# Kernel optimization log

Hardware: AMD Instinct MI355X
Metric: run time of the kernel (lower is better)

The kernel has to match this reference:

```python
import jax, jax.numpy as jnp
import numpy as np

N_POINTS = 1_500_000
N_SUPERPOINTS = 50_000
FEAT_DIM = 32
HIDDEN_DIM = 64
EMBED_DIM = 128


def setup_inputs() -> dict:
    key = jax.random.key(0)
    k1, k2, k3, k4, k5, k6 = jax.random.split(key, 6)
    return {
        "full_features": jax.random.normal(k1, (N_POINTS, FEAT_DIM), dtype=jnp.float32),
        "super_indices": jax.random.randint(k2, (N_POINTS,), 0, N_SUPERPOINTS, dtype=jnp.int64)
        if jax.config.jax_enable_x64 else jax.random.randint(k2, (N_POINTS,), 0, N_SUPERPOINTS, dtype=jnp.int32),
        "W1": jax.random.normal(k3, (FEAT_DIM, HIDDEN_DIM), dtype=jnp.float32) * 0.1,
        "b1": jax.random.normal(k4, (HIDDEN_DIM,), dtype=jnp.float32) * 0.01,
        "W2": jax.random.normal(k5, (HIDDEN_DIM, EMBED_DIM), dtype=jnp.float32) * 0.1,
        "b2": jax.random.normal(k6, (EMBED_DIM,), dtype=jnp.float32) * 0.01,
    }


def reference(full_features, super_indices, W1, b1, W2, b2):
    # Fused gather -> 2-layer MLP -> per-superpoint max reduction.
    # Equivalent to SuperPointNet.gen_token_embed, vectorized over all
    # superpoints instead of a Python loop with boolean-mask gathers.
    h = jax.nn.relu(full_features @ W1 + b1)          # [N, HIDDEN]
    h = jax.nn.relu(h @ W2 + b2)                      # [N, EMBED]
    sp_features = jax.ops.segment_max(
        h, super_indices, num_segments=N_SUPERPOINTS, indices_are_sorted=False
    )                                                  # [NS, EMBED]
    # Guard empty superpoints (segment_max yields -inf); original loop
    # assumes every superpoint id is present.
    sp_features = jnp.where(jnp.isfinite(sp_features), sp_features, 0.0)
    return sp_features
```

## Files before the change

kernel.cpp:

```cpp
#include <hip/hip_runtime.h>
#include <hip/hip_bf16.h>


#define NPTS 1500000
#define NSEG 50000
#define CAP  120
#define CAPX 64

typedef __attribute__((ext_vector_type(8))) short short8;
typedef __attribute__((ext_vector_type(4))) float floatx4;
typedef __attribute__((ext_vector_type(2))) float floatx2;
typedef __attribute__((ext_vector_type(4))) unsigned int uintx4;

__device__ __forceinline__ unsigned short f2bf(float f) {
    unsigned int x = __float_as_uint(f);
    x += 0x7FFFu + ((x >> 16) & 1u);
    return (unsigned short)(x >> 16);
}
__device__ __forceinline__ float bf2f(unsigned short b) {
    return __uint_as_float(((unsigned int)b) << 16);
}
__device__ __forceinline__ unsigned cvt_pk_bf16(float lo, float hi) {
    unsigned r;
    asm("v_cvt_pk_bf16_f32 %0, %1, %2" : "=v"(r) : "v"(lo), "v"(hi));
    return r;
}

__device__ __forceinline__ short8 load_x(const void* Xv, int pid, int quad, int isbf)
{
    if (isbf) {
        return *(const short8*)((const unsigned short*)Xv + (size_t)pid * 32 + quad * 8);
    } else {
        const float* xf = (const float*)Xv + (size_t)pid * 32 + quad * 8;
        const floatx4 f0 = *(const floatx4*)xf;
        const floatx4 f1 = *(const floatx4*)(xf + 4);
        union { short8 s; unsigned u[4]; } a;
        a.u[0] = cvt_pk_bf16(f0[0], f0[1]);
        a.u[1] = cvt_pk_bf16(f0[2], f0[3]);
        a.u[2] = cvt_pk_bf16(f1[0], f1[1]);
        a.u[3] = cvt_pk_bf16(f1[2], f1[3]);
        return a.s;
    }
}

__device__ __forceinline__ int probe_idx64(const unsigned* idxw, unsigned* scnt)
{
    __syncthreads();
    if (threadIdx.x == 0) *scnt = 0u;
    __syncthreads();
    int nz = 0;
    #pragma unroll
    for (int j = 0; j < 2; ++j)
        nz += (idxw[(threadIdx.x * 2 + j) * 2 + 1] != 0u) ? 1 : 0;
    atomicAdd(scnt, (unsigned)nz);
    __syncthreads();
    return (*scnt < 256u) ? 1 : 0;
}

__device__ __forceinline__ int probe_isbf(const unsigned* Xw, unsigned* scnt)
{
    __syncthreads();
    if (threadIdx.x == 0) *scnt = 0u;
    __syncthreads();
    int c = 0;
    #pragma unroll
    for (int j = 0; j < 4; ++j) {
        unsigned u  = Xw[threadIdx.x * 4 + j];
        unsigned he = (u >> 23) & 0xFFu, le = (u >> 7) & 0xFFu;
        c += (he >= 100u && he <= 140u && le >= 100u && le <= 140u) ? 1 : 0;
    }
    atomicAdd(scnt, (unsigned)c);
    __syncthreads();
    return (*scnt >= 512u) ? 1 : 0;
}

__device__ __forceinline__ void load_row(const unsigned* Xw, int i, int isbf, uintx4 r[4])
{
    if (isbf) {
        const uintx4* s = (const uintx4*)((const char*)Xw + (size_t)i * 64);
        r[0] = s[0]; r[1] = s[1]; r[2] = s[2]; r[3] = s[3];
    } else {
        const floatx4* f = (const floatx4*)((const char*)Xw + (size_t)i * 128);
        #pragma unroll
        for (int k = 0; k < 4; ++k) {
            const floatx4 a = f[2 * k], b = f[2 * k + 1];
            uintx4 w;
            w[0] = cvt_pk_bf16(a[0], a[1]);
            w[1] = cvt_pk_bf16(a[2], a[3]);
            w[2] = cvt_pk_bf16(b[0], b[1]);
            w[3] = cvt_pk_bf16(b[2], b[3]);
            r[k] = w;
        }
    }
}

__global__ __launch_bounds__(256)
void build_rows(const unsigned* __restrict__ idxw,
                const unsigned* __restrict__ Xw,
                unsigned* __restrict__ cnt,
                int* __restrict__ slots,
                unsigned short* __restrict__ Xs,
                unsigned* __restrict__ flags)
{
    __shared__ unsigned sc;
    const int idx64 = probe_idx64(idxw, &sc);
    const int isbf  = probe_isbf(Xw, &sc);
    if (blockIdx.x == 0 && threadIdx.x == 0) flags[0] = (unsigned)isbf;

    const int S  = gridDim.x * 256;
    const int i0 = blockIdx.x * 256 + threadIdx.x;
    const int i1 = i0 + S;

    unsigned s0 = 0xFFFFFFFFu, s1 = 0xFFFFFFFFu;
    if (i0 < NPTS) s0 = idx64 ? idxw[2 * (size_t)i0] : idxw[i0];
    if (i1 < NPTS) s1 = idx64 ? idxw[2 * (size_t)i1] : idxw[i1];

    uintx4 r0[4], r1[4];
    if (s0 < NSEG) load_row(Xw, i0, isbf, r0);
    if (s1 < NSEG) load_row(Xw, i1, isbf, r1);

    unsigned p0 = 0, p1 = 0;
    if (s0 < NSEG) p0 = atomicAdd(&cnt[s0], 1u);
    if (s1 < NSEG) p1 = atomicAdd(&cnt[s1], 1u);

    if (s0 < NSEG) {
        if (p0 < CAP)  slots[(size_t)s0 * CAP + p0] = i0;
        if (p0 < CAPX) {
            uintx4* d = (uintx4*)(Xs + ((size_t)s0 * CAPX + p0) * 32);
            d[0] = r0[0]; d[1] = r0[1]; d[2] = r0[2]; d[3] = r0[3];
        }
    }
    if (s1 < NSEG) {
        if (p1 < CAP)  slots[(size_t)s1 * CAP + p1] = i1;
        if (p1 < CAPX) {
            uintx4* d = (uintx4*)(Xs + ((size_t)s1 * CAPX + p1) * 32);
            d[0] = r1[0]; d[1] = r1[1]; d[2] = r1[2]; d[3] = r1[3];
        }
    }
}

__device__ __forceinline__ void tile_mlp(const short8 acur,
                                         const short8 w1f[4],
                                         const short8 w2f[2][8],
                                         const float b1v[16],
                                         const float b2v[8],
                                         float vmax[8],
                                         const int quad,
                                         const int lim, const bool full)
{
    floatx4 c1[4];
    #pragma unroll
    for (int t = 0; t < 4; ++t) {
        floatx4 z = {0.f, 0.f, 0.f, 0.f};
        c1[t] = __builtin_amdgcn_mfma_f32_16x16x32_bf16(w1f[t], acur, z, 0, 0, 0);
    }

    union { short8 s; unsigned u[4]; } af0, af1;
    #pragma unroll
    for (int t = 0; t < 4; ++t) {
        const float h0 = fmaxf(c1[t][0] + b1v[t * 4 + 0], 0.f);
        const float h1 = fmaxf(c1[t][1] + b1v[t * 4 + 1], 0.f);
        const float h2 = fmaxf(c1[t][2] + b1v[t * 4 + 2], 0.f);
        const float h3 = fmaxf(c1[t][3] + b1v[t * 4 + 3], 0.f);
        const unsigned lo = cvt_pk_bf16(h0, h1);
        const unsigned hi = cvt_pk_bf16(h2, h3);
        if (t == 0)      { af0.u[0] = lo; af0.u[1] = hi; }
        else if (t == 1) { af0.u[2] = lo; af0.u[3] = hi; }
        else if (t == 2) { af1.u[0] = lo; af1.u[1] = hi; }
        else             { af1.u[2] = lo; af1.u[3] = hi; }
    }

    #pragma unroll
    for (int t = 0; t < 8; ++t) {
        floatx4 c4 = {0.f, 0.f, 0.f, 0.f};
        c4 = __builtin_amdgcn_mfma_f32_16x16x32_bf16(af0.s, w2f[0][t], c4, 0, 0, 0);
        c4 = __builtin_amdgcn_mfma_f32_16x16x32_bf16(af1.s, w2f[1][t], c4, 0, 0, 0);
        #pragma unroll
        for (int r = 0; r < 4; ++r) {
            const float v = c4[r] + b2v[t];
            vmax[t] = fmaxf(vmax[t], (full || (quad * 4 + r) < lim) ? v : 0.f);
        }
    }
}

__device__ __forceinline__ short8 row_tile(const unsigned short* Xs, int seg,
                                           int ti, int l16, int quad)
{
    return *(const short8*)(Xs + ((size_t)seg * CAPX + ti * 16 + l16) * 32 + quad * 8);
}

template<int DT>
__global__ __launch_bounds__(256)
void seg_mlp_rows(const void* __restrict__ Xv,
                  const void* __restrict__ W1v, const void* __restrict__ B1v,
                  const void* __restrict__ W2v, const void* __restrict__ B2v,
                  const unsigned* __restrict__ cnt,
                  const int* __restrict__ slots,
                  const unsigned short* __restrict__ Xs,
                  const unsigned* __restrict__ flags,
                  void* __restrict__ outv)
{
    if (flags[0] != (unsigned)DT) return;

    __shared__ __align__(16) float outs[4][128];

    const int tid = threadIdx.x, wave = tid >> 6, lane = tid & 63;
    const int quad = lane >> 4, l16 = lane & 15;

    short8 w1f[4];
    #pragma unroll
    for (int t = 0; t < 4; ++t)
        #pragma unroll
        for (int j = 0; j < 8; ++j) {
            const int e = (quad * 8 + j) * 64 + t * 16 + l16;
            w1f[t][j] = DT ? (short)((const unsigned short*)W1v)[e]
                           : (short)f2bf(((const float*)W1v)[e]);
        }

    short8 w2f[2][8];
    #pragma unroll
    for (int kt = 0; kt < 2; ++kt)
        #pragma unroll
        for (int t = 0; t < 8; ++t)
            #pragma unroll
            for (int j = 0; j < 8; ++j) {
                const int k = kt * 32 + (j >> 2) * 16 + quad * 4 + (j & 3);
                const int e = k * 128 + t * 16 + l16;
                w2f[kt][t][j] = DT ? (short)((const unsigned short*)W2v)[e]
                                   : (short)f2bf(((const float*)W2v)[e]);
            }

    float b1v[16];
    #pragma unroll
    for (int t = 0; t < 4; ++t)
        #pragma unroll
        for (int r = 0; r < 4; ++r) {
            const int n = t * 16 + quad * 4 + r;
            b1v[t * 4 + r] = DT ? bf2f(((const unsigned short*)B1v)[n])
                                : ((const float*)B1v)[n];
        }
    float b2v[8];
    #pragma unroll
    for (int t = 0; t < 8; ++t)
        b2v[t] = DT ? bf2f(((const unsigned short*)B2v)[t * 16 + l16])
                    : ((const float*)B2v)[t * 16 + l16];

    float* fs = outs[wave];
    const int gw = blockIdx.x * 4 + wave, nw = gridDim.x * 4;

    unsigned c_cur = 0;
    short8 r0 = {}, r1 = {};
    if (gw < NSEG) {
        c_cur = cnt[gw];
        r0 = row_tile(Xs, gw, 0, l16, quad);
        r1 = row_tile(Xs, gw, 1, l16, quad);
    }

    for (int seg = gw; seg < NSEG; seg += nw) {
        const int c_raw = (int)c_cur;
        const int c  = min(c_raw, CAPX);
        const int nt = (c + 15) >> 4;

        short8 r2 = {}, r3 = {};
        if (nt > 2) r2 = row_tile(Xs, seg, 2, l16, quad);
        if (nt > 3) r3 = row_tile(Xs, seg, 3, l16, quad);

        const int segn = seg + nw;
        unsigned cn = 0;
        short8 r0n = {}, r1n = {};
        if (segn < NSEG) {
            cn  = cnt[segn];
            r0n = row_tile(Xs, segn, 0, l16, quad);
            r1n = row_tile(Xs, segn, 1, l16, quad);
        }

        float vmax[8];
        #pragma unroll
        for (int t = 0; t < 8; ++t) vmax[t] = 0.f;

        if (c_raw > CAPX) {
            const int c2 = min(c_raw, CAP);
            const int nt2 = (c2 + 15) >> 4, last = c2 - 1;
            const size_t base = (size_t)seg * CAP;
            for (int ti = 0; ti < nt2; ++ti) {
                int pid = slots[base + min(ti * 16 + l16, last)];
                pid = min(max(pid, 0), NPTS - 1);
                const short8 acur = load_x(Xv, pid, quad, DT);
                tile_mlp(acur, w1f, w2f, b1v, b2v, vmax, quad, 16, true);
            }
        } else if (c > 0) {
            #pragma unroll
            for (int ti = 0; ti < 4; ++ti) {
                if (ti < nt) {
                    const short8 acur = (ti == 0) ? r0 : (ti == 1) ? r1
                                      : (ti == 2) ? r2 : r3;
                    const int lim = c - ti * 16;
                    tile_mlp(acur, w1f, w2f, b1v, b2v, vmax, quad,
                             lim, lim >= 16);
                }
            }
        }

        #pragma unroll
        for (int t = 0; t < 8; ++t) {
            vmax[t] = fmaxf(vmax[t], __shfl_xor(vmax[t], 16, 64));
            vmax[t] = fmaxf(vmax[t], __shfl_xor(vmax[t], 32, 64));
        }
        if (quad == 0) {
            #pragma unroll
            for (int t = 0; t < 8; ++t) fs[t * 16 + l16] = vmax[t];
        }
        __builtin_amdgcn_s_waitcnt(0xC07F);
        const floatx2 o2 = ((const floatx2*)fs)[lane];
        if (DT) {
            ((unsigned*)outv)[seg * 64 + lane] = cvt_pk_bf16(o2[0], o2[1]);
        } else {
            ((floatx2*)outv)[seg * 64 + lane] = o2;
        }
        __builtin_amdgcn_s_waitcnt(0xC07F);

        c_cur = cn; r0 = r0n; r1 = r1n;
    }
}

__global__ __launch_bounds__(256)
void build_slots(const unsigned* __restrict__ idxw,
                 const unsigned* __restrict__ Xw,
                 unsigned* __restrict__ cnt,
                 int* __restrict__ slots,
                 unsigned* __restrict__ flags)
{
    __shared__ unsigned sc;
    const int idx64 = probe_idx64(idxw, &sc);

    if (blockIdx.x == 0) {
        const int isbf = probe_isbf(Xw, &sc);
        if (threadIdx.x == 0) flags[0] = (unsigned)isbf;
    }

    const int S  = gridDim.x * 256;
    const int i0 = blockIdx.x * 256 + threadIdx.x;
    const int i1 = i0 + S, i2 = i1 + S;

    unsigned s0 = 0xFFFFFFFFu, s1 = 0xFFFFFFFFu, s2 = 0xFFFFFFFFu;
    if (i0 < NPTS) s0 = idx64 ? idxw[2 * (size_t)i0] : idxw[i0];
    if (i1 < NPTS) s1 = idx64 ? idxw[2 * (size_t)i1] : idxw[i1];
    if (i2 < NPTS) s2 = idx64 ? idxw[2 * (size_t)i2] : idxw[i2];

    unsigned p0 = 0, p1 = 0, p2 = 0;
    if (s0 < NSEG) p0 = atomicAdd(&cnt[s0], 1u);
    if (s1 < NSEG) p1 = atomicAdd(&cnt[s1], 1u);
    if (s2 < NSEG) p2 = atomicAdd(&cnt[s2], 1u);

    if (s0 < NSEG && p0 < CAP) slots[(size_t)s0 * CAP + p0] = i0;
    if (s1 < NSEG && p1 < CAP) slots[(size_t)s1 * CAP + p1] = i1;
    if (s2 < NSEG && p2 < CAP) slots[(size_t)s2 * CAP + p2] = i2;
}

template<int DT>
__global__ __launch_bounds__(256)
void seg_mlp_max(const void* __restrict__ Xv,
                 const void* __restrict__ W1v, const void* __restrict__ B1v,
                 const void* __restrict__ W2v, const void* __restrict__ B2v,
                 const unsigned* __restrict__ cnt,
                 const int* __restrict__ slots,
                 const unsigned* __restrict__ flags,
                 void* __restrict__ outv)
{
    if (flags[0] != (unsigned)DT) return;

    __shared__ __align__(16) float outs[4][128];

    const int tid = threadIdx.x, wave = tid >> 6, lane = tid & 63;
    const int quad = lane >> 4, l16 = lane & 15;

    short8 w1f[4];
    #pragma unroll
    for (int t = 0; t < 4; ++t)
        #pragma unroll
        for (int j = 0; j < 8; ++j) {
            const int e = (quad * 8 + j) * 64 + t * 16 + l16;
            w1f[t][j] = DT ? (short)((const unsigned short*)W1v)[e]
                           : (short)f2bf(((const float*)W1v)[e]);
        }
    short8 w2f[2][8];
    #pragma unroll
    for (int kt = 0; kt < 2; ++kt)
        #pragma unroll
        for (int t = 0; t < 8; ++t)
            #pragma unroll
            for (int j = 0; j < 8; ++j) {
                const int k = kt * 32 + (j >> 2) * 16 + quad * 4 + (j & 3);
                const int e = k * 128 + t * 16 + l16;
                w2f[kt][t][j] = DT ? (short)((const unsigned short*)W2v)[e]
                                   : (short)f2bf(((const float*)W2v)[e]);
            }
    float b1v[16];
    #pragma unroll
    for (int t = 0; t < 4; ++t)
        #pragma unroll
        for (int r = 0; r < 4; ++r) {
            const int n = t * 16 + quad * 4 + r;
            b1v[t * 4 + r] = DT ? bf2f(((const unsigned short*)B1v)[n])
                                : ((const float*)B1v)[n];
        }
    float b2v[8];
    #pragma unroll
    for (int t = 0; t < 8; ++t)
        b2v[t] = DT ? bf2f(((const unsigned short*)B2v)[t * 16 + l16])
                    : ((const float*)B2v)[t * 16 + l16];

    float* fs = outs[wave];
    const int gw = blockIdx.x * 4 + wave, nw = gridDim.x * 4;

    for (int seg = gw; seg < NSEG; seg += nw) {
        const int c = min((int)cnt[seg], CAP);

        float vmax[8];
        #pragma unroll
        for (int t = 0; t < 8; ++t) vmax[t] = 0.f;

        if (c > 0) {
            const int nt = (c + 15) >> 4, last = c - 1;
            const size_t base = (size_t)seg * CAP;

            short8 abuf[2];
            abuf[0] = load_x(Xv, slots[base + min(l16, last)], quad, DT);
            if (nt > 1)
                abuf[1] = load_x(Xv, slots[base + min(16 + l16, last)], quad, DT);

            for (int ti = 0; ti < nt; ++ti) {
                const short8 acur = abuf[ti & 1];
                if (ti + 2 < nt)
                    abuf[ti & 1] = load_x(
                        Xv, slots[base + min((ti + 2) * 16 + l16, last)], quad, DT);
                tile_mlp(acur, w1f, w2f, b1v, b2v, vmax, quad, 16, true);
            }
        }

        #pragma unroll
        for (int t = 0; t < 8; ++t) {
            vmax[t] = fmaxf(vmax[t], __shfl_xor(vmax[t], 16, 64));
            vmax[t] = fmaxf(vmax[t], __shfl_xor(vmax[t], 32, 64));
        }
        if (quad == 0) {
            #pragma unroll
            for (int t = 0; t < 8; ++t) fs[t * 16 + l16] = vmax[t];
        }
        __builtin_amdgcn_s_waitcnt(0xC07F);
        const floatx2 o2 = ((const floatx2*)fs)[lane];
        if (DT) {
            ((unsigned*)outv)[seg * 64 + lane] = cvt_pk_bf16(o2[0], o2[1]);
        } else {
            ((floatx2*)outv)[seg * 64 + lane] = o2;
        }
        __builtin_amdgcn_s_waitcnt(0xC07F);
    }
}

extern "C" void kernel_launch(void* const* d_in, const int* in_sizes, int n_in,
                              void* d_out, int out_size, void* d_ws, size_t ws_size,
                              hipStream_t stream)
{
    const void* X   = d_in[0];
    const void* idx = d_in[1];
    const void* W1  = d_in[2];
    const void* B1  = d_in[3];
    const void* W2  = d_in[4];
    const void* B2  = d_in[5];

    char* w = (char*)d_ws;
    unsigned* cnt   = (unsigned*)w;  w += ((size_t)NSEG * 4 + 63) & ~63ull;
    unsigned* flags = (unsigned*)w;  w += 64;
    int*      slots = (int*)w;       w += (size_t)NSEG * CAP * 4;
    unsigned short* Xs = (unsigned short*)w;

    const size_t need_fast =
        (((size_t)NSEG * 4 + 63) & ~63ull) + 64 +
        (size_t)NSEG * CAP * 4 + (size_t)NSEG * CAPX * 64;

    hipMemsetAsync(cnt, 0, (size_t)NSEG * 4, stream);

    if (ws_size >= need_fast) {
        build_rows<<<3072, 256, 0, stream>>>((const unsigned*)idx, (const unsigned*)X,
                                             cnt, slots, Xs, flags);
        seg_mlp_rows<1><<<4096, 256, 0, stream>>>(X, W1, B1, W2, B2, cnt, slots,
                                                  Xs, flags, d_out);
        seg_mlp_rows<0><<<4096, 256, 0, stream>>>(X, W1, B1, W2, B2, cnt, slots,
                                                  Xs, flags, d_out);
    } else {
        build_slots<<<2048, 256, 0, stream>>>((const unsigned*)idx, (const unsigned*)X,
                                              cnt, slots, flags);
        seg_mlp_max<1><<<4096, 256, 0, stream>>>(X, W1, B1, W2, B2, cnt, slots,
                                                 flags, d_out);
        seg_mlp_max<0><<<4096, 256, 0, stream>>>(X, W1, B1, W2, B2, cnt, slots,
                                                 flags, d_out);
    }
}
```

Baseline: 449.3 us.

## Pad per-segment counters to 128B lines and prefetch all four row tiles

Segment counters are spread so each occupies its own 128-byte line, so the atomic increments in the scatter kernel no longer hit the same cache line as neighbouring segments. The MLP kernel now prefetches all four staged row tiles of the next segment unconditionally, instead of two tiles ahead plus two on demand, to hide load latency. The cost is a larger workspace and a bigger counter memset, plus extra loads of unused tiles for small segments.

Result: no change. 456.3 us (+1.5%).

```diff
diff --git a/kernel.cpp b/kernel.cpp
--- a/kernel.cpp
+++ b/kernel.cpp
@@ -100,7 +100,8 @@
                 unsigned* __restrict__ cnt,
                 int* __restrict__ slots,
                 unsigned short* __restrict__ Xs,
-                unsigned* __restrict__ flags)
+                unsigned* __restrict__ flags,
+                const int csh)
 {
     __shared__ unsigned sc;
     const int idx64 = probe_idx64(idxw, &sc);
@@ -120,8 +121,8 @@
     if (s1 < NSEG) load_row(Xw, i1, isbf, r1);
 
     unsigned p0 = 0, p1 = 0;
-    if (s0 < NSEG) p0 = atomicAdd(&cnt[s0], 1u);
-    if (s1 < NSEG) p1 = atomicAdd(&cnt[s1], 1u);
+    if (s0 < NSEG) p0 = atomicAdd(&cnt[(size_t)s0 << csh], 1u);
+    if (s1 < NSEG) p1 = atomicAdd(&cnt[(size_t)s1 << csh], 1u);
 
     if (s0 < NSEG) {
         if (p0 < CAP)  slots[(size_t)s0 * CAP + p0] = i0;
@@ -198,7 +199,8 @@
                   const int* __restrict__ slots,
                   const unsigned short* __restrict__ Xs,
                   const unsigned* __restrict__ flags,
-                  void* __restrict__ outv)
+                  void* __restrict__ outv,
+                  const int csh)
 {
     if (flags[0] != (unsigned)DT) return;
 
@@ -249,30 +251,30 @@
     const int gw = blockIdx.x * 4 + wave, nw = gridDim.x * 4;
 
     unsigned c_cur = 0;
-    short8 r0 = {}, r1 = {};
+    short8 t0 = {}, t1 = {}, t2 = {}, t3 = {};
     if (gw < NSEG) {
-        c_cur = cnt[gw];
-        r0 = row_tile(Xs, gw, 0, l16, quad);
-        r1 = row_tile(Xs, gw, 1, l16, quad);
+        c_cur = cnt[(size_t)gw << csh];
+        t0 = row_tile(Xs, gw, 0, l16, quad);
+        t1 = row_tile(Xs, gw, 1, l16, quad);
+        t2 = row_tile(Xs, gw, 2, l16, quad);
+        t3 = row_tile(Xs, gw, 3, l16, quad);
     }
 
     for (int seg = gw; seg < NSEG; seg += nw) {
+        const int segn = seg + nw;
+        unsigned cn = 0;
+        short8 n0 = {}, n1 = {}, n2 = {}, n3 = {};
+        if (segn < NSEG) {
+            cn = cnt[(size_t)segn << csh];
+            n0 = row_tile(Xs, segn, 0, l16, quad);
+            n1 = row_tile(Xs, segn, 1, l16, quad);
+            n2 = row_tile(Xs, segn, 2, l16, quad);
+            n3 = row_tile(Xs, segn, 3, l16, quad);
+        }
+
         const int c_raw = (int)c_cur;
         const int c  = min(c_raw, CAPX);
         const int nt = (c + 15) >> 4;
-
-        short8 r2 = {}, r3 = {};
-        if (nt > 2) r2 = row_tile(Xs, seg, 2, l16, quad);
-        if (nt > 3) r3 = row_tile(Xs, seg, 3, l16, quad);
-
-        const int segn = seg + nw;
-        unsigned cn = 0;
-        short8 r0n = {}, r1n = {};
-        if (segn < NSEG) {
-            cn  = cnt[segn];
-            r0n = row_tile(Xs, segn, 0, l16, quad);
-            r1n = row_tile(Xs, segn, 1, l16, quad);
-        }
 
         float vmax[8];
         #pragma unroll
@@ -292,8 +294,8 @@
             #pragma unroll
             for (int ti = 0; ti < 4; ++ti) {
                 if (ti < nt) {
-                    const short8 acur = (ti == 0) ? r0 : (ti == 1) ? r1
-                                      : (ti == 2) ? r2 : r3;
+                    const short8 acur = (ti == 0) ? t0 : (ti == 1) ? t1
+                                      : (ti == 2) ? t2 : t3;
                     const int lim = c - ti * 16;
                     tile_mlp(acur, w1f, w2f, b1v, b2v, vmax, quad,
                              lim, lim >= 16);
@@ -319,7 +321,7 @@
         }
         __builtin_amdgcn_s_waitcnt(0xC07F);
 
-        c_cur = cn; r0 = r0n; r1 = r1n;
+        c_cur = cn; t0 = n0; t1 = n1; t2 = n2; t3 = n3;
     }
 }
 
@@ -469,26 +471,38 @@
     const void* W2  = d_in[4];
     const void* B2  = d_in[5];
 
-    char* w = (char*)d_ws;
-    unsigned* cnt   = (unsigned*)w;  w += ((size_t)NSEG * 4 + 63) & ~63ull;
-    unsigned* flags = (unsigned*)w;  w += 64;
-    int*      slots = (int*)w;       w += (size_t)NSEG * CAP * 4;
-    unsigned short* Xs = (unsigned short*)w;
-
-    const size_t need_fast =
-        (((size_t)NSEG * 4 + 63) & ~63ull) + 64 +
-        (size_t)NSEG * CAP * 4 + (size_t)NSEG * CAPX * 64;
-
-    hipMemsetAsync(cnt, 0, (size_t)NSEG * 4, stream);
-
-    if (ws_size >= need_fast) {
+    const size_t slots_sz = (size_t)NSEG * CAP * 4;
+    const size_t xs_sz    = (size_t)NSEG * CAPX * 64;
+    const size_t cnt_pad  = (size_t)NSEG * 128;
+    const size_t cnt_base = ((size_t)NSEG * 4 + 63) & ~63ull;
+
+    const size_t need_pad  = cnt_pad  + 64 + slots_sz + xs_sz;
+    const size_t need_base = cnt_base + 64 + slots_sz + xs_sz;
+
+    if (ws_size >= need_base) {
+        const int    csh    = (ws_size >= need_pad) ? 5 : 0;
+        const size_t cnt_sz = (csh == 5) ? cnt_pad : cnt_base;
+
+        char* w = (char*)d_ws;
+        unsigned* cnt   = (unsigned*)w;  w += cnt_sz;
+        unsigned* flags = (unsigned*)w;  w += 64;
+        int*      slots = (int*)w;       w += slots_sz;
+        unsigned short* Xs = (unsigned short*)w;
+
+        hipMemsetAsync(cnt, 0, (size_t)NSEG * 4 << csh, stream);
         build_rows<<<3072, 256, 0, stream>>>((const unsigned*)idx, (const unsigned*)X,
-                                             cnt, slots, Xs, flags);
+                                             cnt, slots, Xs, flags, csh);
         seg_mlp_rows<1><<<4096, 256, 0, stream>>>(X, W1, B1, W2, B2, cnt, slots,
-                                                  Xs, flags, d_out);
+                                                  Xs, flags, d_out, csh);
         seg_mlp_rows<0><<<4096, 256, 0, stream>>>(X, W1, B1, W2, B2, cnt, slots,
-                                                  Xs, flags, d_out);
+                                                  Xs, flags, d_out, csh);
     } else {
+        char* w = (char*)d_ws;
+        unsigned* cnt   = (unsigned*)w;  w += cnt_base;
+        unsigned* flags = (unsigned*)w;  w += 64;
+        int*      slots = (int*)w;
+
+        hipMemsetAsync(cnt, 0, (size_t)NSEG * 4, stream);
         build_slots<<<2048, 256, 0, stream>>>((const unsigned*)idx, (const unsigned*)X,
                                               cnt, slots, flags);
         seg_mlp_max<1><<<4096, 256, 0, stream>>>(X, W1, B1, W2, B2, cnt, slots,
```
